# Performance work log

Measured on AMD Instinct MI355X. Metric: run time of the kernel, lower is better.

The kernel has to match this reference:

```python
import jax, jax.numpy as jnp
import numpy as np

DECAY = 0.99
EPS = 1e-5
K = 1024  # num_embeddings
D = 64    # embedding_dim


def setup_inputs() -> dict:
    key = jax.random.key(0)
    k1, k2 = jax.random.split(key)
    inputs = jax.random.normal(k1, (64, 64, 32, 32), dtype=jnp.float32)
    weight = jax.random.uniform(k2, (K, D), minval=-1.0 / K, maxval=1.0 / K, dtype=jnp.float32)
    cluster_size = jnp.zeros((K,), dtype=jnp.float32)
    embed_avg = weight.copy()
    return {"inputs": inputs, "weight": weight, "cluster_size": cluster_size, "embed_avg": embed_avg}


def reference(inputs, weight, cluster_size, embed_avg):
    B, _, H, W = inputs.shape
    # faithful to torch: raw memory-order view(-1, D), no channel permute
    flat = inputs.reshape(-1, D)  # (N, D), N = B*H*W
    distances = (jnp.sum(flat * flat, axis=1, keepdims=True)
                 + jnp.sum(weight * weight, axis=1)
                 - 2.0 * flat @ weight.T)
    idx = jnp.argmin(distances, axis=1)  # (N,)
    quantized = weight[idx].reshape(inputs.shape)  # == onehot @ weight, reshaped

    # EMA codebook update (training path)
    counts = jax.ops.segment_sum(jnp.ones(flat.shape[0], dtype=jnp.float32), idx, num_segments=K)
    cs = DECAY * cluster_size + (1.0 - DECAY) * counts
    n = jnp.sum(cs)
    cs = (cs + EPS) / (n + K * EPS) * n
    dw = jax.ops.segment_sum(flat, idx, num_segments=K)  # == onehot^T @ flat
    new_embed_avg = DECAY * embed_avg + (1.0 - DECAY) * dw
    new_weight = new_embed_avg / cs[:, None]

    # straight-through estimator
    quantized_st = inputs + jax.lax.stop_gradient(quantized - inputs)
    indices = idx.reshape(B, H, W)
    return quantized_st, indices, new_weight, cs, new_embed_avg
```

## Files before the change

kernel.cpp:

```cpp
#include <hip/hip_runtime.h>

#define NROWS 65536
#define KC    1024
#define DD    64

#define QOFF  0
#define IOFF  4194304
#define WOFF  4259840
#define CSOFF 4325376
#define EAOFF 4326400

#define WS_CODESQ  0
#define WS_COUNTS  1056
#define WS_RCCNT   2080
#define WS_CURSOR  2096
#define WS_OFFS    3120
#define WS_CSFIN   4144
#define WS_DW      5168
#define WS_WSWZ    70704
#define WS_IDX     137264
#define WS_RCLIST  202800
#define WS_ROWLIST 268336
#define WS_PACKED  333872

#define MARGIN 5e-5f

typedef _Float16 half8 __attribute__((ext_vector_type(8)));
typedef float    floatx4 __attribute__((ext_vector_type(4)));

struct F4 { float x, y, z, w; };
typedef const __attribute__((address_space(4))) F4    c4F4;
typedef const __attribute__((address_space(4))) float c4f;

__device__ __forceinline__ unsigned f2ord(float f) {
    unsigned u = __float_as_uint(f);
    return (u & 0x80000000u) ? ~u : (u | 0x80000000u);
}

__device__ __forceinline__ float rowsq4(const float4* xv) {
    float4 re, ro;
    re.x = __fmul_rn(xv[0].x, xv[0].x); re.y = __fmul_rn(xv[0].y, xv[0].y);
    re.z = __fmul_rn(xv[0].z, xv[0].z); re.w = __fmul_rn(xv[0].w, xv[0].w);
    ro.x = __fmul_rn(xv[1].x, xv[1].x); ro.y = __fmul_rn(xv[1].y, xv[1].y);
    ro.z = __fmul_rn(xv[1].z, xv[1].z); ro.w = __fmul_rn(xv[1].w, xv[1].w);
#pragma unroll
    for (int i = 2; i < 16; i += 2) {
        re.x = __fadd_rn(re.x, __fmul_rn(xv[i].x, xv[i].x));
        re.y = __fadd_rn(re.y, __fmul_rn(xv[i].y, xv[i].y));
        re.z = __fadd_rn(re.z, __fmul_rn(xv[i].z, xv[i].z));
        re.w = __fadd_rn(re.w, __fmul_rn(xv[i].w, xv[i].w));
        ro.x = __fadd_rn(ro.x, __fmul_rn(xv[i + 1].x, xv[i + 1].x));
        ro.y = __fadd_rn(ro.y, __fmul_rn(xv[i + 1].y, xv[i + 1].y));
        ro.z = __fadd_rn(ro.z, __fmul_rn(xv[i + 1].z, xv[i + 1].z));
        ro.w = __fadd_rn(ro.w, __fmul_rn(xv[i + 1].w, xv[i + 1].w));
    }
    return __fadd_rn(__fadd_rn(__fadd_rn(re.x, re.y), __fadd_rn(re.z, re.w)),
                     __fadd_rn(__fadd_rn(ro.x, ro.y), __fadd_rn(ro.z, ro.w)));
}

__global__ void prep_kernel(const float* __restrict__ weight,
                            float* __restrict__ code_sq,
                            _Float16* __restrict__ wswz,
                            float* __restrict__ counts,
                            int* __restrict__ rccnt) {
    int c = blockIdx.x * blockDim.x + threadIdx.x;
    if (c >= KC) return;
    counts[c] = 0.0f;
    if (c == 0) rccnt[0] = 0;
    float4 wv4[16];
    const float4* pw = reinterpret_cast<const float4*>(weight + (size_t)c * DD);
#pragma unroll
    for (int i = 0; i < 16; ++i) wv4[i] = pw[i];
    code_sq[c] = rowsq4(wv4);
    float w64[64];
#pragma unroll
    for (int i = 0; i < 16; ++i) {
        w64[4 * i] = wv4[i].x; w64[4 * i + 1] = wv4[i].y;
        w64[4 * i + 2] = wv4[i].z; w64[4 * i + 3] = wv4[i].w;
    }
    const int t32 = c >> 5;
    const int s16 = (c >> 4) & 1;
    const int cl  = c & 15;
    const size_t base = (size_t)t32 * 4096 + s16 * 2048 + cl * 8;
#pragma unroll
    for (int q = 0; q < 8; ++q) {
        half8 h, l;
#pragma unroll
        for (int j = 0; j < 8; ++j) {
            float s = w64[q * 8 + j] * 1024.0f;
            _Float16 hh = (_Float16)s;
            h[j] = hh;
            l[j] = (_Float16)(s - (float)hh);
        }
        *reinterpret_cast<half8*>(wswz + base + q * 128)        = h;
        *reinterpret_cast<half8*>(wswz + base + 1024 + q * 128) = l;
    }
}

__global__ __launch_bounds__(256) void vq_scan(
    const float* __restrict__ x_in, const float* __restrict__ code_sq,
    const _Float16* __restrict__ wswz,
    float* __restrict__ out, float* __restrict__ counts,
    int* __restrict__ idxbuf, int* __restrict__ rccnt, int* __restrict__ rclist,
    unsigned long long* __restrict__ packed) {

    __shared__ __align__(16) _Float16 lds_b[2][4096];
    __shared__ float lds_csq[KC];

    const int tid  = threadIdx.x;
    const int lane = tid & 63;
    const int wv   = tid >> 6;
    const int l15  = lane & 15;
    const int g    = lane >> 4;

    const int blockRow0 = blockIdx.x * 128;
    const int waveRow0  = blockRow0 + wv * 32;

#pragma unroll
    for (int i = 0; i < 4; ++i) lds_csq[tid + i * 256] = code_sq[tid + i * 256];

    half8 ah[4], al[4];
#pragma unroll
    for (int t = 0; t < 2; ++t) {
#pragma unroll
        for (int kh = 0; kh < 2; ++kh) {
            const float4* p4 = reinterpret_cast<const float4*>(
                x_in + (size_t)(waveRow0 + t * 16 + l15) * DD + kh * 32 + g * 8);
            float4 v0 = p4[0], v1 = p4[1];
            float vals[8] = {v0.x, v0.y, v0.z, v0.w, v1.x, v1.y, v1.z, v1.w};
            half8 hh, ll;
#pragma unroll
            for (int j = 0; j < 8; ++j) {
                _Float16 h = (_Float16)vals[j];
                hh[j] = h;
                ll[j] = (_Float16)(vals[j] - (float)h);
            }
            ah[t * 2 + kh] = hh;
            al[t * 2 + kh] = ll;
        }
    }

    {
        const float4* s = reinterpret_cast<const float4*>(wswz);
        float4 a0 = s[tid], a1 = s[tid + 256];
        reinterpret_cast<float4*>(lds_b[0])[tid]       = a0;
        reinterpret_cast<float4*>(lds_b[0])[tid + 256] = a1;
    }
    __syncthreads();

    float m1[2][4], m2[2][4];
    int   i1[2][4];
#pragma unroll
    for (int t = 0; t < 2; ++t)
#pragma unroll
        for (int r = 0; r < 4; ++r) { m1[t][r] = INFINITY; m2[t][r] = INFINITY; i1[t][r] = 0; }

    int cur = 0;
    for (int ct = 0; ct < 32; ++ct) {
        float4 r0, r1;
        if (ct < 31) {
            const float4* s = reinterpret_cast<const float4*>(wswz + (size_t)(ct + 1) * 4096);
            r0 = s[tid];
            r1 = s[tid + 256];
        }

        const _Float16* B = lds_b[cur];
#pragma unroll
        for (int s16 = 0; s16 < 2; ++s16) {
            const _Float16* S = B + s16 * 2048;
            half8 bh0 = *reinterpret_cast<const half8*>(S + g * 128 + l15 * 8);
            half8 bh1 = *reinterpret_cast<const half8*>(S + 512 + g * 128 + l15 * 8);
            half8 bl0 = *reinterpret_cast<const half8*>(S + 1024 + g * 128 + l15 * 8);
            half8 bl1 = *reinterpret_cast<const half8*>(S + 1536 + g * 128 + l15 * 8);
            const int code = ct * 32 + s16 * 16 + l15;
            const float csq = lds_csq[code];
#pragma unroll
            for (int t = 0; t < 2; ++t) {
                floatx4 c = {0.f, 0.f, 0.f, 0.f};
                c = __builtin_amdgcn_mfma_f32_16x16x32_f16(al[t * 2 + 0], bh0, c, 0, 0, 0);
                c = __builtin_amdgcn_mfma_f32_16x16x32_f16(al[t * 2 + 1], bh1, c, 0, 0, 0);
                c = __builtin_amdgcn_mfma_f32_16x16x32_f16(ah[t * 2 + 0], bl0, c, 0, 0, 0);
                c = __builtin_amdgcn_mfma_f32_16x16x32_f16(ah[t * 2 + 1], bl1, c, 0, 0, 0);
                c = __builtin_amdgcn_mfma_f32_16x16x32_f16(ah[t * 2 + 0], bh0, c, 0, 0, 0);
                c = __builtin_amdgcn_mfma_f32_16x16x32_f16(ah[t * 2 + 1], bh1, c, 0, 0, 0);
#pragma unroll
                for (int r = 0; r < 4; ++r) {
                    float s = fmaf(c[r], -0x1p-9f, csq);
                    float mo = m1[t][r];
                    m2[t][r] = fminf(fmaxf(s, mo), m2[t][r]);
                    i1[t][r] = (s < mo) ? code : i1[t][r];
                    m1[t][r] = fminf(mo, s);
                }
            }
        }

        if (ct < 31) {
            reinterpret_cast<float4*>(lds_b[cur ^ 1])[tid]       = r0;
            reinterpret_cast<float4*>(lds_b[cur ^ 1])[tid + 256] = r1;
        }
        __syncthreads();
        cur ^= 1;
    }

#pragma unroll
    for (int t = 0; t < 2; ++t)
#pragma unroll
        for (int r = 0; r < 4; ++r)
#pragma unroll
            for (int mk = 1; mk < 16; mk <<= 1) {
                float o1 = __shfl_xor(m1[t][r], mk);
                float o2 = __shfl_xor(m2[t][r], mk);
                int   oi = __shfl_xor(i1[t][r], mk);
                float n2 = fminf(fminf(m2[t][r], o2), fmaxf(m1[t][r], o1));
                bool sel = (o1 < m1[t][r]) || (o1 == m1[t][r] && oi < i1[t][r]);
                m1[t][r] = sel ? o1 : m1[t][r];
                i1[t][r] = sel ? oi : i1[t][r];
                m2[t][r] = n2;
            }

    if (l15 == 0) {
#pragma unroll
        for (int t = 0; t < 2; ++t)
#pragma unroll
            for (int r = 0; r < 4; ++r) {
                int grow = waveRow0 + t * 16 + g * 4 + r;
                if (m2[t][r] - m1[t][r] >= MARGIN) {
                    idxbuf[grow] = i1[t][r];
                    out[IOFF + grow] = (float)i1[t][r];
                    atomicAdd(&counts[i1[t][r]], 1.0f);
                } else {
                    packed[grow] = 0xFFFFFFFFFFFFFFFFull;
                    int pos = atomicAdd(rccnt, 1);
                    rclist[pos] = grow;
                }
            }
    }
}

__global__ __launch_bounds__(256, 4) void vq_recheck(
    const float* __restrict__ x_in, const float* __restrict__ weight,
    const float* __restrict__ code_sq,
    unsigned long long* __restrict__ packed,
    const int* __restrict__ rccnt, const int* __restrict__ rclist) {

    const int nrc = rccnt[0];
    const int nitems = ((nrc + 63) >> 6) * 16;

    const int tid  = threadIdx.x;
    const int lane = tid & 63;
    const int wvu  = __builtin_amdgcn_readfirstlane(tid >> 6);

    for (int item = blockIdx.x; item < nitems; item += gridDim.x) {
        const int rb     = (item >> 4) * 64;
        const int cchunk = item & 15;
        const bool valid = (rb + lane) < nrc;
        const int  grow  = rclist[valid ? rb + lane : rb];

        float4 xv[16];
        const float4* px = reinterpret_cast<const float4*>(x_in + (size_t)grow * DD);
#pragma unroll
        for (int i = 0; i < 16; ++i) xv[i] = px[i];
        const float rs = rowsq4(xv);

        const int k0 = cchunk * 64 + wvu * 16;
        unsigned long long wa = (unsigned long long)(weight + (size_t)k0 * DD);
        unsigned long long ca = (unsigned long long)(code_sq + k0);
        unsigned wal = __builtin_amdgcn_readfirstlane((unsigned)wa);
        unsigned wah = __builtin_amdgcn_readfirstlane((unsigned)(wa >> 32));
        unsigned cal = __builtin_amdgcn_readfirstlane((unsigned)ca);
        unsigned cah = __builtin_amdgcn_readfirstlane((unsigned)(ca >> 32));
        c4F4* wb4 = (c4F4*)(((unsigned long long)wah << 32) | wal);
        c4f*  cb  = (c4f*)(((unsigned long long)cah << 32) | cal);

        float best = INFINITY;
        int bidx = 0x7fffffff;

#pragma unroll 2
        for (int k = 0; k < 16; ++k) {
            float a0 = 0.f, a1 = 0.f, a2 = 0.f, a3 = 0.f;
#pragma unroll
            for (int i = 0; i < 16; ++i) {
                F4 w4;
                w4.x = wb4[k * 16 + i].x;
                w4.y = wb4[k * 16 + i].y;
                w4.z = wb4[k * 16 + i].z;
                w4.w = wb4[k * 16 + i].w;
                a0 += xv[i].x * w4.x;
                a1 += xv[i].y * w4.y;
                a2 += xv[i].z * w4.z;
                a3 += xv[i].w * w4.w;
            }
            float dot = (a0 + a1) + (a2 + a3);
            float csq = cb[k];
            float dst = __fsub_rn(__fadd_rn(rs, csq), __fmul_rn(2.0f, dot));
            int kg = k0 + k;
            if (dst < best) { best = dst; bidx = kg; }
        }

        if (valid) {
            unsigned long long p =
                ((unsigned long long)f2ord(best) << 32) | (unsigned)bidx;
            atomicMin(&packed[grow], p);
        }
    }
}

__global__ void rc_finalize(const unsigned long long* __restrict__ packed,
                            const int* __restrict__ rccnt,
                            const int* __restrict__ rclist,
                            float* __restrict__ out, float* __restrict__ counts,
                            int* __restrict__ idxbuf) {
    int i = blockIdx.x * blockDim.x + threadIdx.x;
    if (i >= rccnt[0]) return;
    int grow = rclist[i];
    int bidx = (int)(packed[grow] & 0xFFFFFFFFull);
    out[IOFF + grow] = (float)bidx;
    idxbuf[grow] = bidx;
    atomicAdd(&counts[bidx], 1.0f);
}

__global__ void offsets_cs_kernel(const float* __restrict__ counts,
                                  const float* __restrict__ cluster_size,
                                  int* __restrict__ offs, int* __restrict__ cursor,
                                  float* __restrict__ out, float* __restrict__ cs_fin) {
    __shared__ int   sc[1024];
    __shared__ float sb[1024];
    int k = threadIdx.x;
    int c = (int)counts[k];
    float ce = 0.99f * cluster_size[k] + 0.01f * counts[k];
    sc[k] = c;
    sb[k] = ce;
    __syncthreads();
    for (int off = 1; off < 1024; off <<= 1) {
        int v = (k >= off) ? sc[k - off] : 0;
        __syncthreads();
        sc[k] += v;
        __syncthreads();
    }
    offs[k] = sc[k] - c;
    cursor[k] = 0;
    for (int off = 512; off > 0; off >>= 1) {
        if (k < off) sb[k] += sb[k + off];
        __syncthreads();
    }
    float n = sb[0];
    float v = ((ce + 1e-5f) / (n + 0.01024f)) * n;
    out[CSOFF + k] = v;
    cs_fin[k] = v;
}

__global__ void scatter_kernel(const int* __restrict__ idxbuf,
                               const int* __restrict__ offs,
                               int* __restrict__ cursor,
                               int* __restrict__ rowlist) {
    int r = blockIdx.x * blockDim.x + threadIdx.x;
    if (r >= NROWS) return;
    int k = idxbuf[r];
    int pos = atomicAdd(&cursor[k], 1);
    rowlist[offs[k] + pos] = r;
}

__global__ void dw_q_kernel(const float* __restrict__ x_in,
                            const float* __restrict__ weight,
                            const float* __restrict__ counts,
                            const int* __restrict__ offs,
                            const int* __restrict__ rowlist,
                            const float* __restrict__ embed_avg,
                            const float* __restrict__ cs_fin,
                            float* __restrict__ out, float* __restrict__ dw) {
    __shared__ float wsh[64];
    __shared__ float part[4][64];

    const int k    = blockIdx.x;
    const int tid  = threadIdx.x;
    const int lane = tid & 63;
    const int wv   = tid >> 6;

    if (tid < 64) wsh[tid] = weight[(size_t)k * DD + tid];
    __syncthreads();

    const int cnt  = (int)counts[k];
    const int base = offs[k];
    const float wk = wsh[lane];

    float acc = 0.f;
    int i = wv;
    for (; i + 12 < cnt; i += 16) {
        int r0 = rowlist[base + i];
        int r1 = rowlist[base + i + 4];
        int r2 = rowlist[base + i + 8];
        int r3 = rowlist[base + i + 12];
        float x0 = x_in[(size_t)r0 * DD + lane];
        float x1 = x_in[(size_t)r1 * DD + lane];
        float x2 = x_in[(size_t)r2 * DD + lane];
        float x3 = x_in[(size_t)r3 * DD + lane];
        out[QOFF + (size_t)r0 * DD + lane] = __fadd_rn(x0, __fsub_rn(wk, x0));
        out[QOFF + (size_t)r1 * DD + lane] = __fadd_rn(x1, __fsub_rn(wk, x1));
        out[QOFF + (size_t)r2 * DD + lane] = __fadd_rn(x2, __fsub_rn(wk, x2));
        out[QOFF + (size_t)r3 * DD + lane] = __fadd_rn(x3, __fsub_rn(wk, x3));
        acc = __fadd_rn(acc, x0);
        acc = __fadd_rn(acc, x1);
        acc = __fadd_rn(acc, x2);
        acc = __fadd_rn(acc, x3);
    }
    for (; i < cnt; i += 4) {
        int r = rowlist[base + i];
        float xq = x_in[(size_t)r * DD + lane];
        out[QOFF + (size_t)r * DD + lane] = __fadd_rn(xq, __fsub_rn(wk, xq));
        acc = __fadd_rn(acc, xq);
    }
    part[wv][lane] = acc;
    __syncthreads();
    if (tid < 64) {
        float s = __fadd_rn(__fadd_rn(part[0][tid], part[1][tid]),
                            __fadd_rn(part[2][tid], part[3][tid]));
        int e = k * DD + tid;
        dw[e] = s;
        float na = 0.99f * embed_avg[e] + 0.01f * s;
        out[EAOFF + e] = na;
        out[WOFF + e] = na / cs_fin[k];
    }
}

extern "C" void kernel_launch(void* const* d_in, const int* in_sizes, int n_in,
                              void* d_out, int out_size, void* d_ws, size_t ws_size,
                              hipStream_t stream) {
    (void)in_sizes; (void)n_in; (void)out_size; (void)ws_size;
    const float* x       = (const float*)d_in[0];
    const float* weight  = (const float*)d_in[1];
    const float* cluster = (const float*)d_in[2];
    const float* eavg    = (const float*)d_in[3];
    float* out = (float*)d_out;
    float* wsf = (float*)d_ws;

    float*    code_sq = wsf + WS_CODESQ;
    float*    counts  = wsf + WS_COUNTS;
    int*      rccnt   = (int*)(wsf + WS_RCCNT);
    int*      cursor  = (int*)(wsf + WS_CURSOR);
    int*      offs    = (int*)(wsf + WS_OFFS);
    float*    cs_fin  = wsf + WS_CSFIN;
    float*    dwbuf   = wsf + WS_DW;
    _Float16* wswz    = (_Float16*)(wsf + WS_WSWZ);
    int*      idxbuf  = (int*)(wsf + WS_IDX);
    int*      rclist  = (int*)(wsf + WS_RCLIST);
    int*      rowlist = (int*)(wsf + WS_ROWLIST);
    unsigned long long* packed = (unsigned long long*)(wsf + WS_PACKED);

    hipLaunchKernelGGL(prep_kernel, dim3(16), dim3(64), 0, stream,
                       weight, code_sq, wswz, counts, rccnt);
    hipLaunchKernelGGL(vq_scan, dim3(512), dim3(256), 0, stream,
                       x, code_sq, wswz, out, counts, idxbuf, rccnt, rclist,
                       packed);
    hipLaunchKernelGGL(vq_recheck, dim3(2048), dim3(256), 0, stream,
                       x, weight, code_sq, packed, rccnt, rclist);
    hipLaunchKernelGGL(rc_finalize, dim3(256), dim3(256), 0, stream,
                       packed, rccnt, rclist, out, counts, idxbuf);
    hipLaunchKernelGGL(offsets_cs_kernel, dim3(1), dim3(1024), 0, stream,
                       counts, cluster, offs, cursor, out, cs_fin);
    hipLaunchKernelGGL(scatter_kernel, dim3(256), dim3(256), 0, stream,
                       idxbuf, offs, cursor, rowlist);
    hipLaunchKernelGGL(dw_q_kernel, dim3(1024), dim3(256), 0, stream,
                       x, weight, counts, offs, rowlist, eavg, cs_fin, out, dwbuf);
}
```

Before: 132.9 us.

## Split codebook half-tiles across two wave groups in vq_scan with LDS merge

```diff
diff --git a/kernel.cpp b/kernel.cpp
--- a/kernel.cpp
+++ b/kernel.cpp
@@ -97,7 +97,7 @@
     }
 }
 
-__global__ __launch_bounds__(256) void vq_scan(
+__global__ __launch_bounds__(512, 4) void vq_scan(
     const float* __restrict__ x_in, const float* __restrict__ code_sq,
     const _Float16* __restrict__ wswz,
     float* __restrict__ out, float* __restrict__ counts,
@@ -106,18 +106,24 @@
 
     __shared__ __align__(16) _Float16 lds_b[2][4096];
     __shared__ float lds_csq[KC];
+    __shared__ float sm1[8][32], sm2[8][32];
+    __shared__ int   si1[8][32];
 
     const int tid  = threadIdx.x;
     const int lane = tid & 63;
-    const int wv   = tid >> 6;
+    const int w    = tid >> 6;
+    const int wm   = w & 3;
+    const int wsel = w >> 2;
     const int l15  = lane & 15;
     const int g    = lane >> 4;
 
     const int blockRow0 = blockIdx.x * 128;
-    const int waveRow0  = blockRow0 + wv * 32;
-
-#pragma unroll
-    for (int i = 0; i < 4; ++i) lds_csq[tid + i * 256] = code_sq[tid + i * 256];
+    const int waveRow0  = blockRow0 + wm * 32;
+
+    if (tid < 512) {
+        lds_csq[tid] = code_sq[tid];
+        lds_csq[tid + 512] = code_sq[tid + 512];
+    }
 
     half8 ah[4], al[4];
 #pragma unroll
@@ -140,12 +146,8 @@
         }
     }
 
-    {
-        const float4* s = reinterpret_cast<const float4*>(wswz);
-        float4 a0 = s[tid], a1 = s[tid + 256];
-        reinterpret_cast<float4*>(lds_b[0])[tid]       = a0;
-        reinterpret_cast<float4*>(lds_b[0])[tid + 256] = a1;
-    }
+    reinterpret_cast<float4*>(lds_b[0])[tid] =
+        reinterpret_cast<const float4*>(wswz)[tid];
     __syncthreads();
 
     float m1[2][4], m2[2][4];
@@ -157,47 +159,38 @@
 
     int cur = 0;
     for (int ct = 0; ct < 32; ++ct) {
-        float4 r0, r1;
-        if (ct < 31) {
-            const float4* s = reinterpret_cast<const float4*>(wswz + (size_t)(ct + 1) * 4096);
-            r0 = s[tid];
-            r1 = s[tid + 256];
-        }
-
-        const _Float16* B = lds_b[cur];
-#pragma unroll
-        for (int s16 = 0; s16 < 2; ++s16) {
-            const _Float16* S = B + s16 * 2048;
-            half8 bh0 = *reinterpret_cast<const half8*>(S + g * 128 + l15 * 8);
-            half8 bh1 = *reinterpret_cast<const half8*>(S + 512 + g * 128 + l15 * 8);
-            half8 bl0 = *reinterpret_cast<const half8*>(S + 1024 + g * 128 + l15 * 8);
-            half8 bl1 = *reinterpret_cast<const half8*>(S + 1536 + g * 128 + l15 * 8);
-            const int code = ct * 32 + s16 * 16 + l15;
-            const float csq = lds_csq[code];
-#pragma unroll
-            for (int t = 0; t < 2; ++t) {
-                floatx4 c = {0.f, 0.f, 0.f, 0.f};
-                c = __builtin_amdgcn_mfma_f32_16x16x32_f16(al[t * 2 + 0], bh0, c, 0, 0, 0);
-                c = __builtin_amdgcn_mfma_f32_16x16x32_f16(al[t * 2 + 1], bh1, c, 0, 0, 0);
-                c = __builtin_amdgcn_mfma_f32_16x16x32_f16(ah[t * 2 + 0], bl0, c, 0, 0, 0);
-                c = __builtin_amdgcn_mfma_f32_16x16x32_f16(ah[t * 2 + 1], bl1, c, 0, 0, 0);
-                c = __builtin_amdgcn_mfma_f32_16x16x32_f16(ah[t * 2 + 0], bh0, c, 0, 0, 0);
-                c = __builtin_amdgcn_mfma_f32_16x16x32_f16(ah[t * 2 + 1], bh1, c, 0, 0, 0);
-#pragma unroll
-                for (int r = 0; r < 4; ++r) {
-                    float s = fmaf(c[r], -0x1p-9f, csq);
-                    float mo = m1[t][r];
-                    m2[t][r] = fminf(fmaxf(s, mo), m2[t][r]);
-                    i1[t][r] = (s < mo) ? code : i1[t][r];
-                    m1[t][r] = fminf(mo, s);
-                }
-            }
-        }
-
-        if (ct < 31) {
-            reinterpret_cast<float4*>(lds_b[cur ^ 1])[tid]       = r0;
-            reinterpret_cast<float4*>(lds_b[cur ^ 1])[tid + 256] = r1;
-        }
+        float4 r0;
+        if (ct < 31)
+            r0 = reinterpret_cast<const float4*>(wswz + (size_t)(ct + 1) * 4096)[tid];
+
+        const _Float16* S = lds_b[cur] + wsel * 2048;
+        half8 bh0 = *reinterpret_cast<const half8*>(S + g * 128 + l15 * 8);
+        half8 bh1 = *reinterpret_cast<const half8*>(S + 512 + g * 128 + l15 * 8);
+        half8 bl0 = *reinterpret_cast<const half8*>(S + 1024 + g * 128 + l15 * 8);
+        half8 bl1 = *reinterpret_cast<const half8*>(S + 1536 + g * 128 + l15 * 8);
+        const int code = ct * 32 + wsel * 16 + l15;
+        const float csq = lds_csq[code];
+#pragma unroll
+        for (int t = 0; t < 2; ++t) {
+            floatx4 c = {0.f, 0.f, 0.f, 0.f};
+            c = __builtin_amdgcn_mfma_f32_16x16x32_f16(al[t * 2 + 0], bh0, c, 0, 0, 0);
+            c = __builtin_amdgcn_mfma_f32_16x16x32_f16(al[t * 2 + 1], bh1, c, 0, 0, 0);
+            c = __builtin_amdgcn_mfma_f32_16x16x32_f16(ah[t * 2 + 0], bl0, c, 0, 0, 0);
+            c = __builtin_amdgcn_mfma_f32_16x16x32_f16(ah[t * 2 + 1], bl1, c, 0, 0, 0);
+            c = __builtin_amdgcn_mfma_f32_16x16x32_f16(ah[t * 2 + 0], bh0, c, 0, 0, 0);
+            c = __builtin_amdgcn_mfma_f32_16x16x32_f16(ah[t * 2 + 1], bh1, c, 0, 0, 0);
+#pragma unroll
+            for (int r = 0; r < 4; ++r) {
+                float s = fmaf(c[r], -0x1p-9f, csq);
+                float mo = m1[t][r];
+                m2[t][r] = fminf(fmaxf(s, mo), m2[t][r]);
+                i1[t][r] = (s < mo) ? code : i1[t][r];
+                m1[t][r] = fminf(mo, s);
+            }
+        }
+
+        if (ct < 31)
+            reinterpret_cast<float4*>(lds_b[cur ^ 1])[tid] = r0;
         __syncthreads();
         cur ^= 1;
     }
@@ -223,17 +216,40 @@
         for (int t = 0; t < 2; ++t)
 #pragma unroll
             for (int r = 0; r < 4; ++r) {
-                int grow = waveRow0 + t * 16 + g * 4 + r;
-                if (m2[t][r] - m1[t][r] >= MARGIN) {
-                    idxbuf[grow] = i1[t][r];
-                    out[IOFF + grow] = (float)i1[t][r];
-                    atomicAdd(&counts[i1[t][r]], 1.0f);
-                } else {
-                    packed[grow] = 0xFFFFFFFFFFFFFFFFull;
-                    int pos = atomicAdd(rccnt, 1);
-                    rclist[pos] = grow;
-                }
-            }
+                int rib = t * 16 + g * 4 + r;
+                sm1[w][rib] = m1[t][r];
+                sm2[w][rib] = m2[t][r];
+                si1[w][rib] = i1[t][r];
+            }
+    }
+    __syncthreads();
+
+    if (tid < 128) {
+        int pwm = tid >> 5;
+        int rib = tid & 31;
+        float bm1 = sm1[pwm][rib], bm2 = sm2[pwm][rib];
+        int bi = si1[pwm][rib];
+        {
+            float v1 = sm1[pwm | 4][rib];
+            float v2 = sm2[pwm | 4][rib];
+            int   vi = si1[pwm | 4][rib];
+            if (v1 < bm1 || (v1 == bm1 && vi < bi)) {
+                bm2 = fminf(bm1, v2);
+                bm1 = v1; bi = vi;
+            } else {
+                bm2 = fminf(bm2, v1);
+            }
+        }
+        int grow = blockRow0 + pwm * 32 + rib;
+        if (bm2 - bm1 >= MARGIN) {
+            idxbuf[grow] = bi;
+            out[IOFF + grow] = (float)bi;
+            atomicAdd(&counts[bi], 1.0f);
+        } else {
+            packed[grow] = 0xFFFFFFFFFFFFFFFFull;
+            int pos = atomicAdd(rccnt, 1);
+            rclist[pos] = grow;
+        }
     }
 }
 
@@ -448,7 +464,7 @@
 
     hipLaunchKernelGGL(prep_kernel, dim3(16), dim3(64), 0, stream,
                        weight, code_sq, wswz, counts, rccnt);
-    hipLaunchKernelGGL(vq_scan, dim3(512), dim3(256), 0, stream,
+    hipLaunchKernelGGL(vq_scan, dim3(512), dim3(512), 0, stream,
                        x, code_sq, wswz, out, counts, idxbuf, rccnt, rclist,
                        packed);
     hipLaunchKernelGGL(vq_recheck, dim3(2048), dim3(256), 0, stream,
```

Result: faster. 121.4 us (-8.6%).
